# Kernel tuning notes

Hardware: AMD Instinct MI355X
Metric: run time of the kernel (lower is better)

The kernel has to match this reference:

```python
import jax, jax.numpy as jnp
import numpy as np

N_TOKEN = 1024
FFN_MULT = 4
B = 32
D = 1024
LN_EPS = 1e-5


def _layer_norm(x, gamma, beta):
    mu = jnp.mean(x, axis=-1, keepdims=True)
    var = jnp.var(x, axis=-1, keepdims=True)
    return (x - mu) * jax.lax.rsqrt(var + LN_EPS) * gamma + beta


def setup_inputs() -> dict:
    key = jax.random.key(0)
    ks = jax.random.split(key, 12)
    n, m = N_TOKEN, FFN_MULT * N_TOKEN
    s_in = 1.0 / np.sqrt(n)
    s_ff = 1.0 / np.sqrt(m)
    return {
        "Q": jax.random.normal(ks[0], (B, n), jnp.float32),
        "K": jax.random.normal(ks[1], (B, n, D), jnp.float32),
        "V": jax.random.normal(ks[2], (B, n, D), jnp.float32),
        "mu_w": jax.random.uniform(ks[3], (n, n), jnp.float32, -s_in, s_in),
        "mu_b": jax.random.uniform(ks[4], (n,), jnp.float32, -s_in, s_in),
        "sigma_w": jax.random.uniform(ks[5], (n, n), jnp.float32, -s_in, s_in),
        "sigma_b": jax.random.uniform(ks[6], (n,), jnp.float32, -s_in, s_in),
        "ffn_w1": jax.random.uniform(ks[7], (m, n), jnp.float32, -s_in, s_in),
        "ffn_b1": jax.random.uniform(ks[8], (m,), jnp.float32, -s_in, s_in),
        "ffn_w2": jax.random.uniform(ks[9], (n, m), jnp.float32, -s_ff, s_ff),
        "ffn_b2": jax.random.uniform(ks[10], (n,), jnp.float32, -s_ff, s_ff),
        "ln_ff_g": jnp.ones((n,), jnp.float32),
        "ln_ff_b": jnp.zeros((n,), jnp.float32),
        "ln_q_g": jnp.ones((n,), jnp.float32),
        "ln_q_b": jnp.zeros((n,), jnp.float32),
    }


def reference(Q, K, V, mu_w, mu_b, sigma_w, sigma_b, ffn_w1, ffn_b1,
              ffn_w2, ffn_b2, ln_ff_g, ln_ff_b, ln_q_g, ln_q_b):
    q = _layer_norm(Q, ln_q_g, ln_q_b)                       # (B, n)
    mu = jnp.tanh(q @ mu_w.T + mu_b)[..., None]              # (B, n, 1)
    sigma = (q @ sigma_w.T + sigma_b)[..., None]             # (B, n, 1)
    # Gaussian-kernel pseudo-attention: broadcast over D then reduce
    S = jnp.exp(-0.5 * (K - mu) ** 2 / (sigma ** 2 + 1e-8))  # (B, n, D)
    A = jnp.sum(S * V, axis=-1)                              # (B, n)
    x = A + Q
    h = _layer_norm(x, ln_ff_g, ln_ff_b)
    h = jax.nn.silu(h @ ffn_w1.T + ffn_b1) @ ffn_w2.T + ffn_b2
    return x + h
```

## Files before the change

kernel.cpp:

```cpp
#include <hip/hip_runtime.h>

#define N_TOK  1024
#define D_DIM  1024
#define M_FFN  4096

typedef float f32x4 __attribute__((ext_vector_type(4)));

__device__ __forceinline__ float wave_reduce(float v) {
    #pragma unroll
    for (int off = 32; off > 0; off >>= 1) v += __shfl_xor(v, off);
    return v;
}

__global__ void ln_kernel(const float* __restrict__ X,
                          const float* __restrict__ gam,
                          const float* __restrict__ bet,
                          float* __restrict__ Y) {
    int b = blockIdx.x, t = threadIdx.x;
    float4 x = ((const float4*)(X + (size_t)b * N_TOK))[t];
    float s = x.x + x.y + x.z + x.w;
    float q = x.x*x.x + x.y*x.y + x.z*x.z + x.w*x.w;
    s = wave_reduce(s); q = wave_reduce(q);
    __shared__ float sa[4], sb[4];
    int wid = t >> 6;
    if ((t & 63) == 0) { sa[wid] = s; sb[wid] = q; }
    __syncthreads();
    float ts = sa[0] + sa[1] + sa[2] + sa[3];
    float tq = sb[0] + sb[1] + sb[2] + sb[3];
    float mean = ts * (1.f / N_TOK);
    float var  = tq * (1.f / N_TOK) - mean * mean;
    float rs = rsqrtf(var + 1e-5f);
    float4 g4 = ((const float4*)gam)[t];
    float4 b4 = ((const float4*)bet)[t];
    float4 o;
    o.x = (x.x - mean) * rs * g4.x + b4.x;
    o.y = (x.y - mean) * rs * g4.y + b4.y;
    o.z = (x.z - mean) * rs * g4.z + b4.z;
    o.w = (x.w - mean) * rs * g4.w + b4.w;
    ((float4*)(Y + (size_t)b * N_TOK))[t] = o;
}

__device__ __forceinline__ void gemm_body(const float* __restrict__ A,
                                          const float* __restrict__ W,
                                          float* __restrict__ C,
                                          const float* __restrict__ bias,
                                          int N, int K, int kchunk, int mode,
                                          int bx, int by) {
    int t = threadIdx.x;
    int lane = t & 63, wid = t >> 6;
    int ksub = lane & 15, nsub = lane >> 4;
    int mhalf = wid & 1, ngrp = wid >> 1;
    int n = bx * 8 + ngrp * 4 + nsub;
    int k0 = by * kchunk + ksub * 4;
    const float* wp = W + (size_t)n * K + k0;
    const float* ap = A + (size_t)mhalf * 16 * K + k0;
    float acc[16];
    #pragma unroll
    for (int j = 0; j < 16; j++) acc[j] = 0.f;
    for (int kk = 0; kk < kchunk; kk += 64) {
        f32x4 w4 = __builtin_nontemporal_load((const f32x4*)(wp + kk));
        #pragma unroll
        for (int j = 0; j < 16; j++) {
            float4 a4 = *(const float4*)(ap + (size_t)j * K + kk);
            acc[j] += a4.x*w4.x + a4.y*w4.y + a4.z*w4.z + a4.w*w4.w;
        }
    }
    #pragma unroll
    for (int j = 0; j < 16; j++) {
        #pragma unroll
        for (int off = 1; off < 16; off <<= 1)
            acc[j] += __shfl_xor(acc[j], off);
    }
    if (ksub == 0) {
        int mbase = mhalf * 16;
        if (mode == 1) {
            float bn = bias[n];
            #pragma unroll
            for (int j = 0; j < 16; j++) {
                float z = acc[j] + bn;
                C[(size_t)(mbase + j) * N + n] = z / (1.f + __expf(-z));
            }
        } else {
            #pragma unroll
            for (int j = 0; j < 16; j++)
                C[(size_t)(mbase + j) * N + n] = acc[j];
        }
    }
}

__global__ void gemm_mu_sigma(const float* __restrict__ A,
                              const float* __restrict__ W0,
                              const float* __restrict__ W1,
                              float* __restrict__ S) {
    const float* W = blockIdx.z ? W1 : W0;
    float* C = S + ((size_t)blockIdx.z * 2 + blockIdx.y) * 32768;
    gemm_body(A, W, C, nullptr, 1024, 1024, 512, 0, blockIdx.x, blockIdx.y);
}

__global__ void gemm_ffn1(const float* __restrict__ A,
                          const float* __restrict__ W,
                          float* __restrict__ C,
                          const float* __restrict__ bias) {
    gemm_body(A, W, C, bias, 4096, 1024, 1024, 1, blockIdx.x, 0);
}

__global__ void gemm_ffn2(const float* __restrict__ A,
                          const float* __restrict__ W,
                          float* __restrict__ S) {
    float* C = S + (size_t)blockIdx.y * 32768;
    gemm_body(A, W, C, nullptr, 1024, 4096, 1024, 0, blockIdx.x, blockIdx.y);
}

__global__ void attn_kernel(const float* __restrict__ Kp,
                            const float* __restrict__ Vp,
                            const float* __restrict__ Qp,
                            const float* __restrict__ MS,
                            const float* __restrict__ mu_b,
                            const float* __restrict__ sg_b,
                            float* __restrict__ xo) {
    int t = threadIdx.x;
    int lane = t & 63, wid = t >> 6;
    int row0 = blockIdx.x * 8 + wid * 2;
    int row1 = row0 + 1;
    const f32x4* kp0 = (const f32x4*)(Kp + (size_t)row0 * D_DIM);
    const f32x4* vp0 = (const f32x4*)(Vp + (size_t)row0 * D_DIM);
    const f32x4* kp1 = (const f32x4*)(Kp + (size_t)row1 * D_DIM);
    const f32x4* vp1 = (const f32x4*)(Vp + (size_t)row1 * D_DIM);
    f32x4 ka[4], va[4], kb[4], vb[4];
    #pragma unroll
    for (int c = 0; c < 4; c++) ka[c] = __builtin_nontemporal_load(kp0 + c * 64 + lane);
    #pragma unroll
    for (int c = 0; c < 4; c++) kb[c] = __builtin_nontemporal_load(kp1 + c * 64 + lane);
    #pragma unroll
    for (int c = 0; c < 4; c++) va[c] = __builtin_nontemporal_load(vp0 + c * 64 + lane);
    #pragma unroll
    for (int c = 0; c < 4; c++) vb[c] = __builtin_nontemporal_load(vp1 + c * 64 + lane);
    int i0 = row0 & (N_TOK - 1), i1 = row1 & (N_TOK - 1);
    float mu0 = tanhf(MS[row0] + MS[row0 + 32768] + mu_b[i0]);
    float mu1 = tanhf(MS[row1] + MS[row1 + 32768] + mu_b[i1]);
    float sg0 = MS[row0 + 65536] + MS[row0 + 98304] + sg_b[i0];
    float sg1 = MS[row1 + 65536] + MS[row1 + 98304] + sg_b[i1];
    float c0 = -0.5f / (sg0 * sg0 + 1e-8f);
    float c1 = -0.5f / (sg1 * sg1 + 1e-8f);
    float acc0 = 0.f, acc1 = 0.f, d;
    #pragma unroll
    for (int c = 0; c < 4; c++) {
        d = ka[c].x - mu0; acc0 += __expf(c0 * d * d) * va[c].x;
        d = ka[c].y - mu0; acc0 += __expf(c0 * d * d) * va[c].y;
        d = ka[c].z - mu0; acc0 += __expf(c0 * d * d) * va[c].z;
        d = ka[c].w - mu0; acc0 += __expf(c0 * d * d) * va[c].w;
        d = kb[c].x - mu1; acc1 += __expf(c1 * d * d) * vb[c].x;
        d = kb[c].y - mu1; acc1 += __expf(c1 * d * d) * vb[c].y;
        d = kb[c].z - mu1; acc1 += __expf(c1 * d * d) * vb[c].z;
        d = kb[c].w - mu1; acc1 += __expf(c1 * d * d) * vb[c].w;
    }
    acc0 = wave_reduce(acc0);
    acc1 = wave_reduce(acc1);
    if (lane == 0) {
        xo[row0] = acc0 + Qp[row0];
        xo[row1] = acc1 + Qp[row1];
    }
}

__global__ void final_kernel(const float* __restrict__ x,
                             const float* __restrict__ F2,
                             const float* __restrict__ b2,
                             float* __restrict__ out) {
    int idx = blockIdx.x * 256 + threadIdx.x;
    float acc = (F2[idx] + F2[idx + 32768]) + (F2[idx + 65536] + F2[idx + 98304]);
    out[idx] = x[idx] + acc + b2[idx & (N_TOK - 1)];
}

extern "C" void kernel_launch(void* const* d_in, const int* in_sizes, int n_in,
                              void* d_out, int out_size, void* d_ws, size_t ws_size,
                              hipStream_t stream) {
    const float* Q       = (const float*)d_in[0];
    const float* Kp      = (const float*)d_in[1];
    const float* Vp      = (const float*)d_in[2];
    const float* mu_w    = (const float*)d_in[3];
    const float* mu_b    = (const float*)d_in[4];
    const float* sigma_w = (const float*)d_in[5];
    const float* sigma_b = (const float*)d_in[6];
    const float* w1      = (const float*)d_in[7];
    const float* b1      = (const float*)d_in[8];
    const float* w2      = (const float*)d_in[9];
    const float* b2      = (const float*)d_in[10];
    const float* ln_ff_g = (const float*)d_in[11];
    const float* ln_ff_b = (const float*)d_in[12];
    const float* ln_q_g  = (const float*)d_in[13];
    const float* ln_q_b  = (const float*)d_in[14];

    float* ms_sl  = (float*)d_ws;
    float* f2_sl  = ms_sl  + 131072;
    float* xbuf   = f2_sl  + 131072;
    float* qln    = xbuf   + 32768;
    float* h0     = qln    + 32768;
    float* g      = h0     + 32768;

    ln_kernel<<<32, 256, 0, stream>>>(Q, ln_q_g, ln_q_b, qln);

    gemm_mu_sigma<<<dim3(128, 2, 2), 256, 0, stream>>>(qln, mu_w, sigma_w, ms_sl);

    attn_kernel<<<4096, 256, 0, stream>>>(Kp, Vp, Q, ms_sl, mu_b, sigma_b, xbuf);

    ln_kernel<<<32, 256, 0, stream>>>(xbuf, ln_ff_g, ln_ff_b, h0);

    gemm_ffn1<<<512, 256, 0, stream>>>(h0, w1, g, b1);

    gemm_ffn2<<<dim3(128, 4), 256, 0, stream>>>(g, w2, f2_sl);
    final_kernel<<<128, 256, 0, stream>>>(xbuf, f2_sl, b2, (float*)d_out);
}
```

Baseline: 370.1 us.

## Fold LayerNorms into the mu/sigma and FFN1 GEMMs algebraically

Drops both standalone LayerNorm launches. Each GEMM block now computes per-row mean and rstd for all 32 rows in shared memory. It then accumulates x·(gamma∘w) along with the row sums of gamma·w and beta·w, and applies the normalization in the epilogue as rs*D - mean*rs*SG + SB. This removes two kernel launches and the normalized intermediate buffers. In exchange, every block rereads the full activation matrix to compute the statistics, and each k-step does extra gamma/beta loads and multiplies.

```diff
diff --git a/kernel.cpp b/kernel.cpp
--- a/kernel.cpp
+++ b/kernel.cpp
@@ -12,39 +12,100 @@
     return v;
 }
 
-__global__ void ln_kernel(const float* __restrict__ X,
-                          const float* __restrict__ gam,
-                          const float* __restrict__ bet,
-                          float* __restrict__ Y) {
-    int b = blockIdx.x, t = threadIdx.x;
-    float4 x = ((const float4*)(X + (size_t)b * N_TOK))[t];
-    float s = x.x + x.y + x.z + x.w;
-    float q = x.x*x.x + x.y*x.y + x.z*x.z + x.w*x.w;
-    s = wave_reduce(s); q = wave_reduce(q);
-    __shared__ float sa[4], sb[4];
-    int wid = t >> 6;
-    if ((t & 63) == 0) { sa[wid] = s; sb[wid] = q; }
+__device__ __forceinline__ void gemm_fln_body(const float* __restrict__ A,
+                                              const float* __restrict__ W,
+                                              float* __restrict__ C,
+                                              const float* __restrict__ bias,
+                                              const float* __restrict__ ln_g,
+                                              const float* __restrict__ ln_b,
+                                              int N, int K, int kchunk, int mode,
+                                              int bx, int by) {
+    __shared__ float s_mean[32], s_rs[32];
+    int t = threadIdx.x;
+    int lane = t & 63, wid = t >> 6;
+
+    #pragma unroll
+    for (int r = 0; r < 8; r++) {
+        int row = wid * 8 + r;
+        const float4* xp = (const float4*)(A + (size_t)row * 1024);
+        float s = 0.f, q = 0.f;
+        #pragma unroll
+        for (int c = 0; c < 4; c++) {
+            float4 x = xp[lane + c * 64];
+            s += x.x + x.y + x.z + x.w;
+            q += x.x*x.x + x.y*x.y + x.z*x.z + x.w*x.w;
+        }
+        s = wave_reduce(s); q = wave_reduce(q);
+        if (lane == 0) {
+            float mean = s * (1.f / 1024.f);
+            float var  = q * (1.f / 1024.f) - mean * mean;
+            s_mean[row] = mean;
+            s_rs[row]   = rsqrtf(var + 1e-5f);
+        }
+    }
     __syncthreads();
-    float ts = sa[0] + sa[1] + sa[2] + sa[3];
-    float tq = sb[0] + sb[1] + sb[2] + sb[3];
-    float mean = ts * (1.f / N_TOK);
-    float var  = tq * (1.f / N_TOK) - mean * mean;
-    float rs = rsqrtf(var + 1e-5f);
-    float4 g4 = ((const float4*)gam)[t];
-    float4 b4 = ((const float4*)bet)[t];
-    float4 o;
-    o.x = (x.x - mean) * rs * g4.x + b4.x;
-    o.y = (x.y - mean) * rs * g4.y + b4.y;
-    o.z = (x.z - mean) * rs * g4.z + b4.z;
-    o.w = (x.w - mean) * rs * g4.w + b4.w;
-    ((float4*)(Y + (size_t)b * N_TOK))[t] = o;
+
+    int ksub = lane & 15, nsub = lane >> 4;
+    int mhalf = wid & 1, ngrp = wid >> 1;
+    int n = bx * 8 + ngrp * 4 + nsub;
+    int k0 = by * kchunk + ksub * 4;
+    const float* wp = W + (size_t)n * K + k0;
+    const float* ap = A + (size_t)(mhalf * 16) * K + k0;
+    const float* gp = ln_g + k0;
+    const float* bp = ln_b + k0;
+    float D[16];
+    #pragma unroll
+    for (int j = 0; j < 16; j++) D[j] = 0.f;
+    float SG = 0.f, SB = 0.f;
+    for (int kk = 0; kk < kchunk; kk += 64) {
+        f32x4 w4 = __builtin_nontemporal_load((const f32x4*)(wp + kk));
+        float4 g4 = *(const float4*)(gp + kk);
+        float4 b4 = *(const float4*)(bp + kk);
+        float gwx = g4.x * w4.x, gwy = g4.y * w4.y,
+              gwz = g4.z * w4.z, gww = g4.w * w4.w;
+        SG += gwx + gwy + gwz + gww;
+        SB += b4.x*w4.x + b4.y*w4.y + b4.z*w4.z + b4.w*w4.w;
+        #pragma unroll
+        for (int j = 0; j < 16; j++) {
+            float4 a4 = *(const float4*)(ap + (size_t)j * K + kk);
+            D[j] += a4.x*gwx + a4.y*gwy + a4.z*gwz + a4.w*gww;
+        }
+    }
+    #pragma unroll
+    for (int j = 0; j < 16; j++) {
+        #pragma unroll
+        for (int off = 1; off < 16; off <<= 1)
+            D[j] += __shfl_xor(D[j], off);
+    }
+    #pragma unroll
+    for (int off = 1; off < 16; off <<= 1) {
+        SG += __shfl_xor(SG, off);
+        SB += __shfl_xor(SB, off);
+    }
+    if (ksub == 0) {
+        int mbase = mhalf * 16;
+        if (mode == 1) {
+            float bn = bias[n];
+            #pragma unroll
+            for (int j = 0; j < 16; j++) {
+                float mean = s_mean[mbase + j], rs = s_rs[mbase + j];
+                float z = rs * D[j] - mean * rs * SG + SB + bn;
+                C[(size_t)(mbase + j) * N + n] = z / (1.f + __expf(-z));
+            }
+        } else {
+            #pragma unroll
+            for (int j = 0; j < 16; j++) {
+                float mean = s_mean[mbase + j], rs = s_rs[mbase + j];
+                C[(size_t)(mbase + j) * N + n] = rs * D[j] - mean * rs * SG + SB;
+            }
+        }
+    }
 }
 
 __device__ __forceinline__ void gemm_body(const float* __restrict__ A,
                                           const float* __restrict__ W,
                                           float* __restrict__ C,
-                                          const float* __restrict__ bias,
-                                          int N, int K, int kchunk, int mode,
+                                          int N, int K, int kchunk,
                                           int bx, int by) {
     int t = threadIdx.x;
     int lane = t & 63, wid = t >> 6;
@@ -73,42 +134,39 @@
     }
     if (ksub == 0) {
         int mbase = mhalf * 16;
-        if (mode == 1) {
-            float bn = bias[n];
-            #pragma unroll
-            for (int j = 0; j < 16; j++) {
-                float z = acc[j] + bn;
-                C[(size_t)(mbase + j) * N + n] = z / (1.f + __expf(-z));
-            }
-        } else {
-            #pragma unroll
-            for (int j = 0; j < 16; j++)
-                C[(size_t)(mbase + j) * N + n] = acc[j];
-        }
-    }
-}
-
-__global__ void gemm_mu_sigma(const float* __restrict__ A,
+        #pragma unroll
+        for (int j = 0; j < 16; j++)
+            C[(size_t)(mbase + j) * N + n] = acc[j];
+    }
+}
+
+__global__ void gemm_mu_sigma(const float* __restrict__ Q,
                               const float* __restrict__ W0,
                               const float* __restrict__ W1,
+                              const float* __restrict__ ln_g,
+                              const float* __restrict__ ln_b,
                               float* __restrict__ S) {
     const float* W = blockIdx.z ? W1 : W0;
     float* C = S + ((size_t)blockIdx.z * 2 + blockIdx.y) * 32768;
-    gemm_body(A, W, C, nullptr, 1024, 1024, 512, 0, blockIdx.x, blockIdx.y);
-}
-
-__global__ void gemm_ffn1(const float* __restrict__ A,
+    gemm_fln_body(Q, W, C, nullptr, ln_g, ln_b,
+                  1024, 1024, 512, 0, blockIdx.x, blockIdx.y);
+}
+
+__global__ void gemm_ffn1(const float* __restrict__ X,
                           const float* __restrict__ W,
+                          const float* __restrict__ ln_g,
+                          const float* __restrict__ ln_b,
                           float* __restrict__ C,
                           const float* __restrict__ bias) {
-    gemm_body(A, W, C, bias, 4096, 1024, 1024, 1, blockIdx.x, 0);
+    gemm_fln_body(X, W, C, bias, ln_g, ln_b,
+                  4096, 1024, 1024, 1, blockIdx.x, 0);
 }
 
 __global__ void gemm_ffn2(const float* __restrict__ A,
                           const float* __restrict__ W,
                           float* __restrict__ S) {
     float* C = S + (size_t)blockIdx.y * 32768;
-    gemm_body(A, W, C, nullptr, 1024, 4096, 1024, 0, blockIdx.x, blockIdx.y);
+    gemm_body(A, W, C, 1024, 4096, 1024, blockIdx.x, blockIdx.y);
 }
 
 __global__ void attn_kernel(const float* __restrict__ Kp,
@@ -193,19 +251,14 @@
     float* ms_sl  = (float*)d_ws;
     float* f2_sl  = ms_sl  + 131072;
     float* xbuf   = f2_sl  + 131072;
-    float* qln    = xbuf   + 32768;
-    float* h0     = qln    + 32768;
-    float* g      = h0     + 32768;
-
-    ln_kernel<<<32, 256, 0, stream>>>(Q, ln_q_g, ln_q_b, qln);
-
-    gemm_mu_sigma<<<dim3(128, 2, 2), 256, 0, stream>>>(qln, mu_w, sigma_w, ms_sl);
+    float* g      = xbuf   + 32768;
+
+    gemm_mu_sigma<<<dim3(128, 2, 2), 256, 0, stream>>>(
+        Q, mu_w, sigma_w, ln_q_g, ln_q_b, ms_sl);
 
     attn_kernel<<<4096, 256, 0, stream>>>(Kp, Vp, Q, ms_sl, mu_b, sigma_b, xbuf);
 
-    ln_kernel<<<32, 256, 0, stream>>>(xbuf, ln_ff_g, ln_ff_b, h0);
-
-    gemm_ffn1<<<512, 256, 0, stream>>>(h0, w1, g, b1);
+    gemm_ffn1<<<512, 256, 0, stream>>>(xbuf, w1, ln_ff_g, ln_ff_b, g, b1);
 
     gemm_ffn2<<<dim3(128, 4), 256, 0, stream>>>(g, w2, f2_sl);
     final_kernel<<<128, 256, 0, stream>>>(xbuf, f2_sl, b2, (float*)d_out);
```

After: 376.5 us. About the same (+1.7%).
